# Kernel tuning notes

Measured on AMD Instinct MI355X. Metric: run time of the kernel, lower is better.

Reference implementation:

```python
import jax, jax.numpy as jnp
import numpy as np

H = 16  # n_heads

def _split_heads(x, n_heads):
    B, S, Dm = x.shape
    return x.reshape(B, S, n_heads, Dm // n_heads).transpose(0, 2, 1, 3)  # [B,H,S,D]

def _matmul_prefix_sum(x, y, z):
    """Faithful, efficient form of the TF matmul_prefix_sum.
    TF builds yz[s] = y[s] (x) z[s] outer products, cumsums over s, then
    contracts with x[t]/ (t+1).  That equals a causal-masked bilinear form:
      out[t, j] = (1/(t+1)) * sum_{s<=t} (x[t]. y[s]) * z[s, j]
    so we compute (x y^T * tril / idx) @ z without the 5D intermediate.
    """
    S = x.shape[2]
    idx = jnp.arange(1, S + 1, dtype=x.dtype)[:, None]        # position 1..S
    mask = jnp.tril(jnp.ones((S, S), dtype=x.dtype))
    scores = jnp.einsum('bhtd,bhsd->bhts', x, y) * (mask / idx)
    return jnp.einsum('bhts,bhsj->bhtj', scores, z)

def setup_inputs() -> dict:
    key = jax.random.key(0)
    ks = jax.random.split(key, 12)
    B, S, Dm = 2, 1024, 1024
    f32 = jnp.float32
    rn = lambda k, shp: jax.random.normal(k, shp, dtype=f32)
    w_scale = f32(1.0 / np.sqrt(Dm))
    return {
        'v': rn(ks[0], (B, S, Dm)),
        'k': rn(ks[1], (B, S, Dm)),
        'q': rn(ks[2], (B, S, Dm)),
        'p': rn(ks[3], (B, S, Dm)),
        'wq_k': rn(ks[4], (Dm, Dm)) * w_scale, 'wq_b': jnp.zeros((Dm,), f32),
        'wk_k': rn(ks[5], (Dm, Dm)) * w_scale, 'wk_b': jnp.zeros((Dm,), f32),
        'wv_k': rn(ks[6], (Dm, Dm)) * w_scale, 'wv_b': jnp.zeros((Dm,), f32),
        'wc_k': rn(ks[7], (Dm, Dm)) * w_scale, 'wc_b': jnp.zeros((Dm,), f32),
    }

def reference(v, k, q, p, wq_k, wq_b, wk_k, wk_b, wv_k, wv_b, wc_k, wc_b):
    B, S, Dm = q.shape
    D = Dm // H
    norm_d = 1.0 / jnp.sqrt(jnp.asarray(D, q.dtype))
    ph = _split_heads(p, H)                                    # [B,H,S,D]
    qh = _split_heads((q @ wq_k + wq_b) * norm_d, H)
    kh = _split_heads(k @ wk_k + wk_b, H)
    vh = _split_heads(v @ wv_k + wv_b, H)
    # elu(p q^T)+1 then transpose -> indexed [B,H,t(query),s(p-position)]
    attn_pack = jax.nn.elu(jnp.einsum('bhtd,bhsd->bhts', qh, ph)) + 1.0
    attn_unpack = _matmul_prefix_sum(qh, kh, attn_pack)        # [B,H,S,S]
    attn_unpack = jax.nn.softmax(attn_unpack, axis=-1)
    attn_out = _matmul_prefix_sum(attn_unpack, attn_pack, vh)  # [B,H,S,D]
    attn_out = attn_out.transpose(0, 2, 1, 3).reshape(B, S, Dm)
    return attn_out @ wc_k + wc_b
```

## Files before the change

### kernel.cpp

```cpp
#include <hip/hip_runtime.h>

#define DEVI static __device__ __forceinline__

using s16x8 = __attribute__((ext_vector_type(8))) short;
using f32x4 = __attribute__((ext_vector_type(4))) float;
using u32x4 = __attribute__((ext_vector_type(4))) unsigned int;

static constexpr int H  = 16;
static constexpr int S  = 1024;
static constexpr int DM = 1024;
static constexpr int NB = 2;
static constexpr int BS = NB * S;
static constexpr long SS  = (long)S * S;
static constexpr long HSS = (long)H * SS;
static constexpr long SDM = (long)S * DM;

DEVI unsigned short f2bf(float f) {
    union { float f; unsigned u; } c; c.f = f;
    c.u += 0x7FFFu + ((c.u >> 16) & 1u);
    return (unsigned short)(c.u >> 16);
}
DEVI float bf2f(unsigned short v) {
    union { unsigned u; float f; } c; c.u = ((unsigned)v) << 16;
    return c.f;
}

DEVI void gload16(const unsigned short* g, unsigned short* l) {
    __builtin_amdgcn_global_load_lds(
        (const __attribute__((address_space(1))) unsigned int*)g,
        (__attribute__((address_space(3))) unsigned int*)l, 16, 0, 0);
}

enum { EPI_BFB = 0, EPI_VTB, EPI_PACK, EPI_MASK, EPI_BF, EPI_OUT };

__global__ __launch_bounds__(256)
void gemmE(const unsigned short* __restrict__ Aall,
           const unsigned short* __restrict__ Ball,
           unsigned short* __restrict__ Oall, float* __restrict__ sums)
{
    const int L = (int)blockIdx.x + ((int)blockIdx.y << 3) + ((int)blockIdx.z << 6);
    const int g = L & 7, r = L >> 3;
    const int bz = g + ((r >> 6) << 3);
    const int bx = r & 7;
    const int by = 7 - ((r >> 3) & 7);
    const int m0 = by * 128, n0 = bx * 128;
    const unsigned short* Ap = Aall + (long)bz * SS;
    const unsigned short* Bp = Ball + (long)bz * SS;

    __shared__ alignas(16) unsigned short lA[128 * 64];
    __shared__ alignas(16) unsigned short lB[128 * 64];

    const int tid = threadIdx.x, w = tid >> 6, lane = tid & 63;
    const int lr = lane & 15, lg = lane >> 4;
    const int wm = (w >> 1) << 6, wn = (w & 1) << 6;

    const unsigned short* gA[4]; const unsigned short* gB[4]; int lo[4];
#pragma unroll
    for (int i = 0; i < 4; ++i) {
        const int q = (i * 4 + w) * 64 + lane, row = q >> 3, slot = q & 7;
        const int gs = (slot ^ (row & 7)) * 8;
        gA[i] = Ap + (long)(m0 + row) * S + gs;
        gB[i] = Bp + (long)(n0 + row) * S + gs;
        lo[i] = (i * 4 + w) * 512;
    }

    int abase[4], axor[4], bbase[4], bxor[4];
#pragma unroll
    for (int f = 0; f < 4; ++f) {
        const int ra = wm + f * 16 + lr;
        abase[f] = ra * 64; axor[f] = (ra & 7) * 8;
        const int rb = wn + f * 16 + lr;
        bbase[f] = rb * 64; bxor[f] = (rb & 7) * 8;
    }

    f32x4 acc[4][4] = {};
    const int Keff = m0 + 128;

    for (int k0 = 0; k0 < Keff; k0 += 64) {
#pragma unroll
        for (int i = 0; i < 4; ++i) {
            gload16(gA[i] + k0, &lA[lo[i]]);
            gload16(gB[i] + k0, &lB[lo[i]]);
        }
        __syncthreads();
#pragma unroll
        for (int kk = 0; kk < 64; kk += 32) {
            s16x8 af[4], bv[4];
#pragma unroll
            for (int f = 0; f < 4; ++f) {
                af[f] = *reinterpret_cast<const s16x8*>(&lA[abase[f] + ((kk + 8 * lg) ^ axor[f])]);
                bv[f] = *reinterpret_cast<const s16x8*>(&lB[bbase[f] + ((kk + 8 * lg) ^ bxor[f])]);
            }
#pragma unroll
            for (int fm = 0; fm < 4; ++fm)
#pragma unroll
                for (int fn = 0; fn < 4; ++fn)
                    acc[fm][fn] = __builtin_amdgcn_mfma_f32_16x16x32_bf16(af[fm], bv[fn], acc[fm][fn], 0, 0, 0);
        }
        __syncthreads();
    }

    const long obase = (long)bz * SS;
#pragma unroll
    for (int fm = 0; fm < 4; ++fm) {
        const int t0 = m0 + wm + fm * 16 + lg * 4;
        float es[4] = {0.f, 0.f, 0.f, 0.f};
#pragma unroll
        for (int fn = 0; fn < 4; ++fn) {
            const int gn = n0 + wn + fn * 16 + lr;
#pragma unroll
            for (int rr = 0; rr < 4; ++rr) {
                const float e = __expf(acc[fm][fn][rr]);
                Oall[obase + (long)(t0 + rr) * S + gn] = f2bf(e);
                es[rr] += e;
            }
        }
#pragma unroll
        for (int rr = 0; rr < 4; ++rr) {
            float s = es[rr];
            s += __shfl_xor(s, 1); s += __shfl_xor(s, 2);
            s += __shfl_xor(s, 4); s += __shfl_xor(s, 8);
            if (lr == 0) atomicAdd(&sums[(long)bz * S + t0 + rr], s);
        }
    }
}

__global__ __launch_bounds__(256)
void gemmZ(const unsigned short* __restrict__ Aall,
           const unsigned short* __restrict__ Ball,
           unsigned short* __restrict__ Oall, const float* __restrict__ sums)
{
    const int L = (int)blockIdx.x + ((int)blockIdx.y << 3) + ((int)blockIdx.z << 6);
    const int g = L & 7, r = L >> 3;
    const int bz = g + ((r >> 6) << 3);
    const int bx = r & 7;
    const int by = 7 - ((r >> 3) & 7);
    const int m0 = by * 128, n0 = bx * 128;
    if (n0 > m0 + 127) return;
    const unsigned short* Ap = Aall + (long)bz * SS;
    const unsigned short* Bp = Ball + (long)bz * SS;

    __shared__ alignas(16) unsigned short lA[128 * 64];
    __shared__ alignas(16) unsigned short lB[128 * 64];

    const int tid = threadIdx.x, w = tid >> 6, lane = tid & 63;
    const int lr = lane & 15, lg = lane >> 4;
    const int wm = (w >> 1) << 6, wn = (w & 1) << 6;

    const unsigned short* gA[4]; const unsigned short* gB[4]; int lo[4];
#pragma unroll
    for (int i = 0; i < 4; ++i) {
        const int q = (i * 4 + w) * 64 + lane, row = q >> 3, slot = q & 7;
        const int gs = (slot ^ (row & 7)) * 8;
        gA[i] = Ap + (long)(m0 + row) * S + gs;
        gB[i] = Bp + (long)(n0 + row) * S + gs;
        lo[i] = (i * 4 + w) * 512;
    }

    int abase[4], axor[4], bbase[4], bxor[4];
#pragma unroll
    for (int f = 0; f < 4; ++f) {
        const int ra = wm + f * 16 + lr;
        abase[f] = ra * 64; axor[f] = (ra & 7) * 8;
        const int rb = wn + f * 16 + lr;
        bbase[f] = rb * 64; bxor[f] = (rb & 7) * 8;
    }

    f32x4 acc[4][4] = {};

    for (int k0 = 0; k0 < S; k0 += 64) {
#pragma unroll
        for (int i = 0; i < 4; ++i) {
            gload16(gA[i] + k0, &lA[lo[i]]);
            gload16(gB[i] + k0, &lB[lo[i]]);
        }
        __syncthreads();
#pragma unroll
        for (int kk = 0; kk < 64; kk += 32) {
            s16x8 af[4], bv[4];
#pragma unroll
            for (int f = 0; f < 4; ++f) {
                af[f] = *reinterpret_cast<const s16x8*>(&lA[abase[f] + ((kk + 8 * lg) ^ axor[f])]);
                bv[f] = *reinterpret_cast<const s16x8*>(&lB[bbase[f] + ((kk + 8 * lg) ^ bxor[f])]);
            }
#pragma unroll
            for (int fm = 0; fm < 4; ++fm)
#pragma unroll
                for (int fn = 0; fn < 4; ++fn)
                    acc[fm][fn] = __builtin_amdgcn_mfma_f32_16x16x32_bf16(af[fm], bv[fn], acc[fm][fn], 0, 0, 0);
        }
        __syncthreads();
    }

    const long obase = (long)bz * SS;
#pragma unroll
    for (int fm = 0; fm < 4; ++fm) {
        const int t0 = m0 + wm + fm * 16 + lg * 4;
        float rec[4];
#pragma unroll
        for (int rr = 0; rr < 4; ++rr)
            rec[rr] = 1.f / (sums[(long)bz * S + t0 + rr] * (float)(t0 + rr + 1));
#pragma unroll
        for (int fn = 0; fn < 4; ++fn) {
            const int gn = n0 + wn + fn * 16 + lr;
#pragma unroll
            for (int rr = 0; rr < 4; ++rr) {
                const int gm = t0 + rr;
                const float vv = (gn <= gm) ? acc[fm][fn][rr] * rec[rr] : 0.f;
                Oall[obase + (long)gm * S + gn] = f2bf(vv);
            }
        }
    }
}

template<int TM, int TN, int EPI, bool CK, bool CS, bool REVY>
__global__ __launch_bounds__((TM/64)*(TN/64)*64)
void gemmT(const unsigned short* __restrict__ Aall, long a_sb, long a_sh, int lda,
           const unsigned short* __restrict__ Ball, long b_sb, long b_sh, int ldb,
           void* __restrict__ Oall, long o_sb, long o_sh, int ldo,
           const float* __restrict__ bias, int bstride, int K, int NV)
{
    constexpr int WN = TN / 64, WM = TM / 64, NWV = WM * WN, NTHR = NWV * 64;
    constexpr int IA = (TM * 8) / NTHR, IB = (TN * 8) / NTHR;
    constexpr int IMX = IA > IB ? IA : IB;

    const int bx = blockIdx.x;
    const int by = REVY ? (int)gridDim.y - 1 - (int)blockIdx.y : (int)blockIdx.y;
    const int bz = blockIdx.z;
    const int m0 = by * TM, n0 = bx * TN;
    if (CS && n0 > m0 + TM - 1) return;
    const int zb = bz >> 4, zh = bz & 15;
    const unsigned short* Ap = Aall + (long)zb * a_sb + (long)zh * a_sh;
    const unsigned short* Bp = Ball + (long)zb * b_sb + (long)zh * b_sh;
    const float* bi = bias + (long)zh * bstride;

    __shared__ alignas(16) unsigned short lA[TM * 64];
    __shared__ alignas(16) unsigned short lB[TN * 64];

    const int tid = threadIdx.x, w = tid >> 6, lane = tid & 63;
    const int lr = lane & 15, lg = lane >> 4;
    const int wm = (w / WN) * 64, wn = (w % WN) * 64;

    const unsigned short* gA[IA]; int loA[IA];
    const unsigned short* gB[IB]; int loB[IB];
#pragma unroll
    for (int i = 0; i < IA; ++i) {
        const int q = i * NTHR + tid, row = q >> 3, slot = q & 7;
        gA[i]  = Ap + (long)(m0 + row) * lda + ((slot ^ (row & 7)) * 8);
        loA[i] = (i * NWV + w) * 512;
    }
#pragma unroll
    for (int i = 0; i < IB; ++i) {
        const int q = i * NTHR + tid, row = q >> 3, slot = q & 7;
        int rb = n0 + row; if (rb >= NV) rb = NV - 1;
        gB[i]  = Bp + (long)rb * ldb + ((slot ^ (row & 7)) * 8);
        loB[i] = (i * NWV + w) * 512;
    }

    int abase[4], axor[4], bbase[4], bxor[4];
#pragma unroll
    for (int f = 0; f < 4; ++f) {
        const int ra = wm + f * 16 + lr;
        abase[f] = ra * 64; axor[f] = (ra & 7) * 8;
        const int rb = wn + f * 16 + lr;
        bbase[f] = rb * 64; bxor[f] = (rb & 7) * 8;
    }

    f32x4 acc[4][4] = {};
    const int Keff = CK ? ((K < m0 + TM) ? K : m0 + TM) : K;

    for (int k0 = 0; k0 < Keff; k0 += 64) {
#pragma unroll
        for (int i = 0; i < IMX; ++i) {
            if (i < IA) gload16(gA[i] + k0, &lA[loA[i]]);
            if (i < IB) gload16(gB[i] + k0, &lB[loB[i]]);
        }
        __syncthreads();
#pragma unroll
        for (int kk = 0; kk < 64; kk += 32) {
            s16x8 af[4], bv[4];
#pragma unroll
            for (int f = 0; f < 4; ++f) {
                af[f] = *reinterpret_cast<const s16x8*>(&lA[abase[f] + ((kk + 8 * lg) ^ axor[f])]);
                bv[f] = *reinterpret_cast<const s16x8*>(&lB[bbase[f] + ((kk + 8 * lg) ^ bxor[f])]);
            }
#pragma unroll
            for (int fm = 0; fm < 4; ++fm)
#pragma unroll
                for (int fn = 0; fn < 4; ++fn)
                    acc[fm][fn] = __builtin_amdgcn_mfma_f32_16x16x32_bf16(af[fm], bv[fn], acc[fm][fn], 0, 0, 0);
        }
        __syncthreads();
    }

    const long obase = (long)zb * o_sb + (long)zh * o_sh;
#pragma unroll
    for (int fm = 0; fm < 4; ++fm)
#pragma unroll
        for (int fn = 0; fn < 4; ++fn) {
            const int t0 = m0 + wm + fm * 16 + lg * 4;
            const int gn = n0 + wn + fn * 16 + lr;
            if (gn >= NV) continue;
#pragma unroll
            for (int r = 0; r < 4; ++r) {
                const int gm = t0 + r;
                float vv = acc[fm][fn][r];
                const long o = obase + (long)gm * ldo + gn;
                if constexpr (EPI == EPI_BFB) {
                    ((unsigned short*)Oall)[o] = f2bf(vv + bi[gn]);
                } else if constexpr (EPI == EPI_VTB) {
                    ((unsigned short*)Oall)[o] = f2bf(vv + bi[gm]);
                } else if constexpr (EPI == EPI_PACK) {
                    vv = vv > 0.f ? vv + 1.f : __expf(vv);
                    ((unsigned short*)Oall)[o] = f2bf(vv);
                } else if constexpr (EPI == EPI_MASK) {
                    vv = (gn <= gm) ? vv / (float)(gm + 1) : 0.f;
                    ((unsigned short*)Oall)[o] = f2bf(vv);
                } else if constexpr (EPI == EPI_BF) {
                    ((unsigned short*)Oall)[o] = f2bf(vv);
                } else {
                    ((float*)Oall)[o] = vv + bi[gn];
                }
            }
        }
}

__global__ __launch_bounds__(256)
void packsqk(const unsigned short* __restrict__ qh,
             const unsigned short* __restrict__ pbf,
             const unsigned short* __restrict__ kh,
             unsigned short* __restrict__ P, unsigned short* __restrict__ PT,
             unsigned short* __restrict__ SQ)
{
    const int L = (int)blockIdx.x + ((int)blockIdx.y << 3) + ((int)blockIdx.z << 6);
    const int g = L & 7, r = L >> 3;
    const int bzz = g + ((r >> 6) << 3);
    const int bx = r & 7, by = 7 - ((r >> 3) & 7);
    const int job = bzz >> 5, zz = bzz & 31;
    const int m0 = by * 128, n0 = bx * 128;
    if (job && n0 > m0 + 127) return;
    const int zb = zz >> 4, zh = zz & 15;
    const unsigned short* Ap = qh + (long)zb * SDM + zh * 64;
    const unsigned short* Bp = (job ? kh : pbf) + (long)zb * SDM + zh * 64;

    __shared__ alignas(16) unsigned short lA[128 * 64];
    __shared__ alignas(16) unsigned short lB[128 * 64];

    const int tid = threadIdx.x, w = tid >> 6, lane = tid & 63;
    const int lr = lane & 15, lg = lane >> 4;
    const int wm = (w >> 1) << 6, wn = (w & 1) << 6;

#pragma unroll
    for (int i = 0; i < 4; ++i) {
        const int q = i * 256 + tid, row = q >> 3, slot = q & 7;
        const int gs = (slot ^ (row & 7)) * 8;
        gload16(Ap + (long)(m0 + row) * DM + gs, &lA[(i * 4 + w) * 512]);
        gload16(Bp + (long)(n0 + row) * DM + gs, &lB[(i * 4 + w) * 512]);
    }
    __syncthreads();

    f32x4 acc[4][4] = {};
#pragma unroll
    for (int kk = 0; kk < 64; kk += 32) {
        s16x8 af[4], bv[4];
#pragma unroll
        for (int f = 0; f < 4; ++f) {
            const int ra = wm + f * 16 + lr;
            af[f] = *reinterpret_cast<const s16x8*>(&lA[ra * 64 + ((kk + 8 * lg) ^ ((ra & 7) * 8))]);
            const int rb = wn + f * 16 + lr;
            bv[f] = *reinterpret_cast<const s16x8*>(&lB[rb * 64 + ((kk + 8 * lg) ^ ((rb & 7) * 8))]);
        }
#pragma unroll
        for (int fm = 0; fm < 4; ++fm)
#pragma unroll
            for (int fn = 0; fn < 4; ++fn)
                acc[fm][fn] = __builtin_amdgcn_mfma_f32_16x16x32_bf16(af[fm], bv[fn], acc[fm][fn], 0, 0, 0);
    }

    const long obase = (long)zz * SS;
#pragma unroll
    for (int fm = 0; fm < 4; ++fm)
#pragma unroll
        for (int fn = 0; fn < 4; ++fn) {
            const int t0 = m0 + wm + fm * 16 + lg * 4;
            const int gn = n0 + wn + fn * 16 + lr;
            if (job == 0) {
                ushort4 pt;
#pragma unroll
                for (int rr = 0; rr < 4; ++rr) {
                    float vv = acc[fm][fn][rr];
                    vv = vv > 0.f ? vv + 1.f : __expf(vv);
                    const unsigned short b = f2bf(vv);
                    P[obase + (long)(t0 + rr) * S + gn] = b;
                    ((unsigned short*)&pt)[rr] = b;
                }
                *reinterpret_cast<ushort4*>(&PT[obase + (long)gn * S + t0]) = pt;
            } else {
#pragma unroll
                for (int rr = 0; rr < 4; ++rr) {
                    const int gm = t0 + rr;
                    float vv = acc[fm][fn][rr];
                    vv = (gn <= gm) ? vv / (float)(gm + 1) : 0.f;
                    SQ[obase + (long)gm * S + gn] = f2bf(vv);
                }
            }
        }
}

__global__ __launch_bounds__(256)
void prep(const float* __restrict__ q_in, const float* __restrict__ k_in,
          const float* __restrict__ v_in, const float* __restrict__ p_in,
          const float* __restrict__ wq, const float* __restrict__ wk,
          const float* __restrict__ wv, const float* __restrict__ wc,
          const float* __restrict__ wqb, const float* __restrict__ wkb,
          unsigned short* __restrict__ qbf, unsigned short* __restrict__ wqT,
          float* __restrict__ bq2, int n4)
{
    const int z = blockIdx.z, bx = blockIdx.x, tid = threadIdx.x;
    if (z < 4) {
        const int i = bx * 256 + tid;
        if (i >= n4) return;
        const float* s = (z == 0) ? q_in : (z == 1) ? k_in : (z == 2) ? v_in : p_in;
        float4 x = reinterpret_cast<const float4*>(s)[i];
        ushort4 o; o.x = f2bf(x.x); o.y = f2bf(x.y); o.z = f2bf(x.z); o.w = f2bf(x.w);
        reinterpret_cast<ushort4*>(qbf + (size_t)z * n4 * 4)[i] = o;
    } else if (z < 8) {
        if (bx >= 256) return;
        __shared__ unsigned short t[64][72];
        const int zz = z - 4;
        const float* src = (zz == 0) ? wq : (zz == 1) ? wk : (zz == 2) ? wv : wc;
        const float scale = (zz == 0) ? 0.125f : 1.0f;
        unsigned short* dst = wqT + (size_t)zz * DM * DM;
        const int r0 = (bx >> 4) * 64, c0 = (bx & 15) * 64;
        const int lrow = tid >> 2, lseg = (tid & 3) << 4;
        const float4* g4 = reinterpret_cast<const float4*>(src + (long)(r0 + lrow) * DM + c0 + lseg);
        alignas(16) unsigned short tmp[16];
#pragma unroll
        for (int qq = 0; qq < 4; ++qq) {
            float4 x = g4[qq];
            tmp[4*qq+0] = f2bf(x.x * scale); tmp[4*qq+1] = f2bf(x.y * scale);
            tmp[4*qq+2] = f2bf(x.z * scale); tmp[4*qq+3] = f2bf(x.w * scale);
        }
#pragma unroll
        for (int j = 0; j < 16; ++j) t[lrow][lseg + j] = tmp[j];
        __syncthreads();
#pragma unroll
        for (int j = 0; j < 16; ++j) tmp[j] = t[lseg + j][lrow];
        unsigned short* d = dst + (long)(c0 + lrow) * DM + r0 + lseg;
        *reinterpret_cast<u32x4*>(d)     = *reinterpret_cast<const u32x4*>(tmp);
        *reinterpret_cast<u32x4*>(d + 8) = *reinterpret_cast<const u32x4*>(tmp + 8);
    } else {
        if (bx >= 4) return;
        const int i = bx * 256 + tid;
        if (i < DM) { bq2[i] = wqb[i] * 0.125f; bq2[DM + i] = wkb[i]; }
    }
}

extern "C" void kernel_launch(void* const* d_in, const int* in_sizes, int n_in,
                              void* d_out, int out_size, void* d_ws, size_t ws_size,
                              hipStream_t stream)
{
    (void)in_sizes; (void)n_in; (void)out_size;
    const float* v_in = (const float*)d_in[0];
    const float* k_in = (const float*)d_in[1];
    const float* q_in = (const float*)d_in[2];
    const float* p_in = (const float*)d_in[3];
    const float* wq   = (const float*)d_in[4];
    const float* wqb  = (const float*)d_in[5];
    const float* wk   = (const float*)d_in[6];
    const float* wkb  = (const float*)d_in[7];
    const float* wvw  = (const float*)d_in[8];
    const float* wvb  = (const float*)d_in[9];
    const float* wc   = (const float*)d_in[10];
    const float* wcb  = (const float*)d_in[11];
    float* out = (float*)d_out;

    char* ws = (char*)d_ws;
    size_t off = 0;
    auto take = [&](size_t n) { char* p = ws + off; off += (n + 255) & ~(size_t)255; return p; };
    unsigned short* qbf = (unsigned short*)take((size_t)BS * DM * 2);
    unsigned short* kbf = (unsigned short*)take((size_t)BS * DM * 2);
    unsigned short* vbf = (unsigned short*)take((size_t)BS * DM * 2);
    unsigned short* pbf = (unsigned short*)take((size_t)BS * DM * 2);
    unsigned short* wqT = (unsigned short*)take((size_t)DM * DM * 2);
    unsigned short* wkT = (unsigned short*)take((size_t)DM * DM * 2);
    unsigned short* wvT = (unsigned short*)take((size_t)DM * DM * 2);
    unsigned short* wcT = (unsigned short*)take((size_t)DM * DM * 2);
    float*          bq2 = (float*)take((size_t)2 * DM * 4);
    float*          sums= (float*)take((size_t)NB * H * S * 4);
    unsigned short* qh  = (unsigned short*)take((size_t)BS * DM * 2);
    unsigned short* kh  = (unsigned short*)take((size_t)BS * DM * 2);
    unsigned short* vhT = (unsigned short*)take((size_t)BS * DM * 2);
    unsigned short* ao  = (unsigned short*)take((size_t)BS * DM * 2);
    const size_t ssz = (size_t)NB * HSS * 2;
    unsigned short* B1 = (unsigned short*)take(ssz);
    unsigned short* B2 = (unsigned short*)take(ssz);
    unsigned short* B3 = (unsigned short*)take(ssz);
    const bool dual = (ws_size >= off + ssz);
    unsigned short* B4 = dual ? (unsigned short*)take(ssz) : nullptr;
    (void)kbf; (void)wkT;

    const int n4 = BS * DM / 4;
    const dim3 b256(256), b128(128);

    hipMemsetAsync(sums, 0, (size_t)NB * H * S * 4, stream);
    prep<<<dim3(n4 / 256, 1, 9), b256, 0, stream>>>(
        q_in, k_in, v_in, p_in, wq, wk, wvw, wc, wqb, wkb, qbf, wqT, bq2, n4);

    gemmT<64,128,EPI_BFB,false,false,false><<<dim3(8, 32, 2), b128, 0, stream>>>(
        qbf, 0, (long)BS*DM, DM,  wqT, 0, (long)DM*DM, DM,  qh, 0, (long)BS*DM, DM,
        bq2, DM, DM, DM);
    gemmT<64,128,EPI_VTB,false,false,false><<<dim3(8, 16, 2), b128, 0, stream>>>(
        wvT, 0, 0, DM,  vbf, 0, SDM, DM,  vhT, 0, (long)DM*S, S,
        wvb, 0, DM, S);

    unsigned short *pbuf, *ptbuf, *sqkbuf, *ebuf, *s2buf;
    if (dual) {
        packsqk<<<dim3(8, 8, 64), b256, 0, stream>>>(qh, pbf, kh, B1, B2, B3);
        pbuf = B1; ptbuf = B2; sqkbuf = B3; ebuf = B4; s2buf = B3;
    } else {
        gemmT<128,128,EPI_PACK,false,false,false><<<dim3(8, 8, 32), b256, 0, stream>>>(
            pbf, SDM, 64, DM,  qh, SDM, 64, DM,  B1, HSS, SS, S,  wvb, 0, 64, S);
        gemmT<128,128,EPI_MASK,false,true,true><<<dim3(8, 8, 32), b256, 0, stream>>>(
            qh, SDM, 64, DM,  kh, SDM, 64, DM,  B2, HSS, SS, S,  wvb, 0, 64, S);
        ptbuf = B1; sqkbuf = B2; ebuf = B3; pbuf = B1; s2buf = B2;
    }
    gemmE<<<dim3(8, 8, 32), b256, 0, stream>>>(sqkbuf, ptbuf, ebuf, sums);
    if (!dual) {
        gemmT<128,128,EPI_PACK,false,false,false><<<dim3(8, 8, 32), b256, 0, stream>>>(
            qh, SDM, 64, DM,  pbf, SDM, 64, DM,  B1, HSS, SS, S,  wvb, 0, 64, S);
    }
    gemmZ<<<dim3(8, 8, 32), b256, 0, stream>>>(ebuf, pbuf, s2buf, sums);
    gemmT<128,64,EPI_BF,true,false,true><<<dim3(1, 8, 32), b128, 0, stream>>>(
        s2buf, HSS, SS, S,  vhT, (long)DM*S, (long)64*S, S,  ao, SDM, 64, DM,
        wvb, 0, S, 64);
    gemmT<64,128,EPI_OUT,false,false,false><<<dim3(8, 32, 1), b128, 0, stream>>>(
        ao, 0, 0, DM,  wcT, 0, 0, DM,  out, 0, 0, DM,  wcb, 0, DM, DM);
}
```

Measured before the change: 315.6 us.

## Replace atomic softmax row sums with separate rowsum kernel and retile attention GEMMs

The exp GEMM no longer accumulates row sums through shuffles and atomics. A separate rowsum_inv kernel rereads the bf16 exp matrix and writes a per-row reciprocal that already includes the 1/(t+1) factor, which also removes the memset. The gemmT template gains an optional L2-friendly block swizzle, an unused dual-output PACK2 epilogue, and a 64x64 tile for the final attention-times-V GEMM. The cost is one extra full read of a large S×S buffer, and row sums are now taken from bf16-rounded values.

```diff
diff --git a/kernel.cpp b/kernel.cpp
--- a/kernel.cpp
+++ b/kernel.cpp
@@ -31,12 +31,12 @@
         (__attribute__((address_space(3))) unsigned int*)l, 16, 0, 0);
 }
 
-enum { EPI_BFB = 0, EPI_VTB, EPI_PACK, EPI_MASK, EPI_BF, EPI_OUT };
+enum { EPI_BFB = 0, EPI_VTB, EPI_PACK, EPI_PACK2, EPI_MASK, EPI_BF, EPI_OUT };
 
 __global__ __launch_bounds__(256)
-void gemmE(const unsigned short* __restrict__ Aall,
+void gemmU(const unsigned short* __restrict__ Aall,
            const unsigned short* __restrict__ Ball,
-           unsigned short* __restrict__ Oall, float* __restrict__ sums)
+           unsigned short* __restrict__ Oall)
 {
     const int L = (int)blockIdx.x + ((int)blockIdx.y << 3) + ((int)blockIdx.z << 6);
     const int g = L & 7, r = L >> 3;
@@ -102,33 +102,21 @@
 
     const long obase = (long)bz * SS;
 #pragma unroll
-    for (int fm = 0; fm < 4; ++fm) {
-        const int t0 = m0 + wm + fm * 16 + lg * 4;
-        float es[4] = {0.f, 0.f, 0.f, 0.f};
+    for (int fm = 0; fm < 4; ++fm)
 #pragma unroll
         for (int fn = 0; fn < 4; ++fn) {
+            const int t0 = m0 + wm + fm * 16 + lg * 4;
             const int gn = n0 + wn + fn * 16 + lr;
 #pragma unroll
-            for (int rr = 0; rr < 4; ++rr) {
-                const float e = __expf(acc[fm][fn][rr]);
-                Oall[obase + (long)(t0 + rr) * S + gn] = f2bf(e);
-                es[rr] += e;
-            }
-        }
-#pragma unroll
-        for (int rr = 0; rr < 4; ++rr) {
-            float s = es[rr];
-            s += __shfl_xor(s, 1); s += __shfl_xor(s, 2);
-            s += __shfl_xor(s, 4); s += __shfl_xor(s, 8);
-            if (lr == 0) atomicAdd(&sums[(long)bz * S + t0 + rr], s);
-        }
-    }
+            for (int rr = 0; rr < 4; ++rr)
+                Oall[obase + (long)(t0 + rr) * S + gn] = f2bf(__expf(acc[fm][fn][rr]));
+        }
 }
 
 __global__ __launch_bounds__(256)
-void gemmZ(const unsigned short* __restrict__ Aall,
+void gemmV(const unsigned short* __restrict__ Aall,
            const unsigned short* __restrict__ Ball,
-           unsigned short* __restrict__ Oall, const float* __restrict__ sums)
+           unsigned short* __restrict__ Oall, const float* __restrict__ inv2)
 {
     const int L = (int)blockIdx.x + ((int)blockIdx.y << 3) + ((int)blockIdx.z << 6);
     const int g = L & 7, r = L >> 3;
@@ -199,7 +187,7 @@
         float rec[4];
 #pragma unroll
         for (int rr = 0; rr < 4; ++rr)
-            rec[rr] = 1.f / (sums[(long)bz * S + t0 + rr] * (float)(t0 + rr + 1));
+            rec[rr] = inv2[(long)bz * S + t0 + rr];
 #pragma unroll
         for (int fn = 0; fn < 4; ++fn) {
             const int gn = n0 + wn + fn * 16 + lr;
@@ -213,20 +201,28 @@
     }
 }
 
-template<int TM, int TN, int EPI, bool CK, bool CS, bool REVY>
+template<int TM, int TN, int EPI, bool CK, bool CS, bool SWZ, bool REVY>
 __global__ __launch_bounds__((TM/64)*(TN/64)*64)
 void gemmT(const unsigned short* __restrict__ Aall, long a_sb, long a_sh, int lda,
            const unsigned short* __restrict__ Ball, long b_sb, long b_sh, int ldb,
-           void* __restrict__ Oall, long o_sb, long o_sh, int ldo,
+           void* __restrict__ Oall, void* __restrict__ O2, long o_sb, long o_sh, int ldo,
            const float* __restrict__ bias, int bstride, int K, int NV)
 {
     constexpr int WN = TN / 64, WM = TM / 64, NWV = WM * WN, NTHR = NWV * 64;
     constexpr int IA = (TM * 8) / NTHR, IB = (TN * 8) / NTHR;
-    constexpr int IMX = IA > IB ? IA : IB;
-
-    const int bx = blockIdx.x;
-    const int by = REVY ? (int)gridDim.y - 1 - (int)blockIdx.y : (int)blockIdx.y;
-    const int bz = blockIdx.z;
+
+    int bx, by, bz;
+    if (SWZ) {
+        const int L = (int)blockIdx.x + ((int)blockIdx.y << 3) + ((int)blockIdx.z << 6);
+        const int g = L & 7, r = L >> 3;
+        bz = g + ((r >> 6) << 3);
+        bx = r & 7;
+        by = 7 - ((r >> 3) & 7);
+    } else {
+        bx = blockIdx.x;
+        by = REVY ? (int)gridDim.y - 1 - (int)blockIdx.y : (int)blockIdx.y;
+        bz = blockIdx.z;
+    }
     const int m0 = by * TM, n0 = bx * TN;
     if (CS && n0 > m0 + TM - 1) return;
     const int zb = bz >> 4, zh = bz & 15;
@@ -271,10 +267,9 @@
 
     for (int k0 = 0; k0 < Keff; k0 += 64) {
 #pragma unroll
-        for (int i = 0; i < IMX; ++i) {
-            if (i < IA) gload16(gA[i] + k0, &lA[loA[i]]);
-            if (i < IB) gload16(gB[i] + k0, &lB[loB[i]]);
-        }
+        for (int i = 0; i < IA; ++i) gload16(gA[i] + k0, &lA[loA[i]]);
+#pragma unroll
+        for (int i = 0; i < IB; ++i) gload16(gB[i] + k0, &lB[loB[i]]);
         __syncthreads();
 #pragma unroll
         for (int kk = 0; kk < 64; kk += 32) {
@@ -301,25 +296,40 @@
             const int t0 = m0 + wm + fm * 16 + lg * 4;
             const int gn = n0 + wn + fn * 16 + lr;
             if (gn >= NV) continue;
-#pragma unroll
-            for (int r = 0; r < 4; ++r) {
-                const int gm = t0 + r;
-                float vv = acc[fm][fn][r];
-                const long o = obase + (long)gm * ldo + gn;
-                if constexpr (EPI == EPI_BFB) {
-                    ((unsigned short*)Oall)[o] = f2bf(vv + bi[gn]);
-                } else if constexpr (EPI == EPI_VTB) {
-                    ((unsigned short*)Oall)[o] = f2bf(vv + bi[gm]);
-                } else if constexpr (EPI == EPI_PACK) {
+            if constexpr (EPI == EPI_PACK2) {
+                ushort4 pt;
+                unsigned short* o1 = (unsigned short*)Oall;
+                unsigned short* o2 = (unsigned short*)O2;
+#pragma unroll
+                for (int r = 0; r < 4; ++r) {
+                    float vv = acc[fm][fn][r];
                     vv = vv > 0.f ? vv + 1.f : __expf(vv);
-                    ((unsigned short*)Oall)[o] = f2bf(vv);
-                } else if constexpr (EPI == EPI_MASK) {
-                    vv = (gn <= gm) ? vv / (float)(gm + 1) : 0.f;
-                    ((unsigned short*)Oall)[o] = f2bf(vv);
-                } else if constexpr (EPI == EPI_BF) {
-                    ((unsigned short*)Oall)[o] = f2bf(vv);
-                } else {
-                    ((float*)Oall)[o] = vv + bi[gn];
+                    const unsigned short b = f2bf(vv);
+                    o1[obase + (long)(t0 + r) * ldo + gn] = b;
+                    ((unsigned short*)&pt)[r] = b;
+                }
+                *reinterpret_cast<ushort4*>(&o2[obase + (long)gn * ldo + t0]) = pt;
+            } else {
+#pragma unroll
+                for (int r = 0; r < 4; ++r) {
+                    const int gm = t0 + r;
+                    float vv = acc[fm][fn][r];
+                    const long o = obase + (long)gm * ldo + gn;
+                    if constexpr (EPI == EPI_BFB) {
+                        ((unsigned short*)Oall)[o] = f2bf(vv + bi[gn]);
+                    } else if constexpr (EPI == EPI_VTB) {
+                        ((unsigned short*)Oall)[o] = f2bf(vv + bi[gm]);
+                    } else if constexpr (EPI == EPI_PACK) {
+                        vv = vv > 0.f ? vv + 1.f : __expf(vv);
+                        ((unsigned short*)Oall)[o] = f2bf(vv);
+                    } else if constexpr (EPI == EPI_MASK) {
+                        vv = (gn <= gm) ? vv / (float)(gm + 1) : 0.f;
+                        ((unsigned short*)Oall)[o] = f2bf(vv);
+                    } else if constexpr (EPI == EPI_BF) {
+                        ((unsigned short*)Oall)[o] = f2bf(vv);
+                    } else {
+                        ((float*)Oall)[o] = vv + bi[gn];
+                    }
                 }
             }
         }
@@ -405,6 +415,24 @@
                 }
             }
         }
+}
+
+__global__ __launch_bounds__(256)
+void rowsum_inv(const unsigned short* __restrict__ E, float* __restrict__ inv2)
+{
+    const int w = threadIdx.x >> 6, lane = threadIdx.x & 63;
+    const long row = (long)blockIdx.x * 4 + w;
+    const u32x4* r4 = reinterpret_cast<const u32x4*>(E + row * S);
+    u32x4 a = r4[lane * 2], b = r4[lane * 2 + 1];
+    float s = 0.f;
+#pragma unroll
+    for (int i = 0; i < 4; ++i) {
+        s += bf2f((unsigned short)(a[i] & 0xFFFF)) + bf2f((unsigned short)(a[i] >> 16));
+        s += bf2f((unsigned short)(b[i] & 0xFFFF)) + bf2f((unsigned short)(b[i] >> 16));
+    }
+#pragma unroll
+    for (int off = 32; off; off >>= 1) s += __shfl_xor(s, off);
+    if (lane == 0) inv2[row] = 1.f / (s * (float)((row & (S - 1)) + 1));
 }
 
 __global__ __launch_bounds__(256)
@@ -487,7 +515,7 @@
     unsigned short* wvT = (unsigned short*)take((size_t)DM * DM * 2);
     unsigned short* wcT = (unsigned short*)take((size_t)DM * DM * 2);
     float*          bq2 = (float*)take((size_t)2 * DM * 4);
-    float*          sums= (float*)take((size_t)NB * H * S * 4);
+    float*          inv = (float*)take((size_t)NB * H * S * 4);
     unsigned short* qh  = (unsigned short*)take((size_t)BS * DM * 2);
     unsigned short* kh  = (unsigned short*)take((size_t)BS * DM * 2);
     unsigned short* vhT = (unsigned short*)take((size_t)BS * DM * 2);
@@ -501,17 +529,16 @@
     (void)kbf; (void)wkT;
 
     const int n4 = BS * DM / 4;
-    const dim3 b256(256), b128(128);
-
-    hipMemsetAsync(sums, 0, (size_t)NB * H * S * 4, stream);
+    const dim3 b256(256), b128(128), b64(64);
+
     prep<<<dim3(n4 / 256, 1, 9), b256, 0, stream>>>(
         q_in, k_in, v_in, p_in, wq, wk, wvw, wc, wqb, wkb, qbf, wqT, bq2, n4);
 
-    gemmT<64,128,EPI_BFB,false,false,false><<<dim3(8, 32, 2), b128, 0, stream>>>(
-        qbf, 0, (long)BS*DM, DM,  wqT, 0, (long)DM*DM, DM,  qh, 0, (long)BS*DM, DM,
+    gemmT<64,128,EPI_BFB,false,false,false,false><<<dim3(8, 32, 2), b128, 0, stream>>>(
+        qbf, 0, (long)BS*DM, DM,  wqT, 0, (long)DM*DM, DM,  qh, nullptr, 0, (long)BS*DM, DM,
         bq2, DM, DM, DM);
-    gemmT<64,128,EPI_VTB,false,false,false><<<dim3(8, 16, 2), b128, 0, stream>>>(
-        wvT, 0, 0, DM,  vbf, 0, SDM, DM,  vhT, 0, (long)DM*S, S,
+    gemmT<64,128,EPI_VTB,false,false,false,false><<<dim3(8, 16, 2), b128, 0, stream>>>(
+        wvT, 0, 0, DM,  vbf, 0, SDM, DM,  vhT, nullptr, 0, (long)DM*S, S,
         wvb, 0, DM, S);
 
     unsigned short *pbuf, *ptbuf, *sqkbuf, *ebuf, *s2buf;
@@ -519,21 +546,22 @@
         packsqk<<<dim3(8, 8, 64), b256, 0, stream>>>(qh, pbf, kh, B1, B2, B3);
         pbuf = B1; ptbuf = B2; sqkbuf = B3; ebuf = B4; s2buf = B3;
     } else {
-        gemmT<128,128,EPI_PACK,false,false,false><<<dim3(8, 8, 32), b256, 0, stream>>>(
-            pbf, SDM, 64, DM,  qh, SDM, 64, DM,  B1, HSS, SS, S,  wvb, 0, 64, S);
-        gemmT<128,128,EPI_MASK,false,true,true><<<dim3(8, 8, 32), b256, 0, stream>>>(
-            qh, SDM, 64, DM,  kh, SDM, 64, DM,  B2, HSS, SS, S,  wvb, 0, 64, S);
+        gemmT<128,128,EPI_PACK,false,false,true,false><<<dim3(8, 8, 32), b256, 0, stream>>>(
+            pbf, SDM, 64, DM,  qh, SDM, 64, DM,  B1, nullptr, HSS, SS, S,  wvb, 0, 64, S);
+        gemmT<128,128,EPI_MASK,false,true,true,false><<<dim3(8, 8, 32), b256, 0, stream>>>(
+            qh, SDM, 64, DM,  kh, SDM, 64, DM,  B2, nullptr, HSS, SS, S,  wvb, 0, 64, S);
         ptbuf = B1; sqkbuf = B2; ebuf = B3; pbuf = B1; s2buf = B2;
     }
-    gemmE<<<dim3(8, 8, 32), b256, 0, stream>>>(sqkbuf, ptbuf, ebuf, sums);
+    gemmU<<<dim3(8, 8, 32), b256, 0, stream>>>(sqkbuf, ptbuf, ebuf);
+    rowsum_inv<<<dim3(NB*H*S/4), b256, 0, stream>>>(ebuf, inv);
     if (!dual) {
-        gemmT<128,128,EPI_PACK,false,false,false><<<dim3(8, 8, 32), b256, 0, stream>>>(
-            qh, SDM, 64, DM,  pbf, SDM, 64, DM,  B1, HSS, SS, S,  wvb, 0, 64, S);
-    }
-    gemmZ<<<dim3(8, 8, 32), b256, 0, stream>>>(ebuf, pbuf, s2buf, sums);
-    gemmT<128,64,EPI_BF,true,false,true><<<dim3(1, 8, 32), b128, 0, stream>>>(
-        s2buf, HSS, SS, S,  vhT, (long)DM*S, (long)64*S, S,  ao, SDM, 64, DM,
+        gemmT<128,128,EPI_PACK,false,false,true,false><<<dim3(8, 8, 32), b256, 0, stream>>>(
+            qh, SDM, 64, DM,  pbf, SDM, 64, DM,  B1, nullptr, HSS, SS, S,  wvb, 0, 64, S);
+    }
+    gemmV<<<dim3(8, 8, 32), b256, 0, stream>>>(ebuf, pbuf, s2buf, inv);
+    gemmT<64,64,EPI_BF,true,false,false,true><<<dim3(1, 16, 32), b64, 0, stream>>>(
+        s2buf, HSS, SS, S,  vhT, (long)DM*S, (long)64*S, S,  ao, nullptr, SDM, 64, DM,
         wvb, 0, S, 64);
-    gemmT<64,128,EPI_OUT,false,false,false><<<dim3(8, 32, 1), b128, 0, stream>>>(
-        ao, 0, 0, DM,  wcT, 0, 0, DM,  out, 0, 0, DM,  wcb, 0, DM, DM);
-}
+    gemmT<64,128,EPI_OUT,false,false,false,false><<<dim3(8, 32, 1), b128, 0, stream>>>(
+        ao, 0, 0, DM,  wcT, 0, 0, DM,  out, nullptr, 0, 0, DM,  wcb, 0, DM, DM);
+}
```

New measurement: 295.0 us. -6.5%, faster.
